# Kernel tuning notes

Measured on AMD Instinct MI355X. Metric: run time of the kernel, lower is better.

The kernel has to match this reference:

```python
import jax, jax.numpy as jnp
import numpy as np

NUM_LATENTS = 1
NUM_EMBEDDINGS = 2048
EMBEDDING_DIM = 64
DECAY = 0.99
EPS = 1e-5


def setup_inputs() -> dict:
    key = jax.random.key(0)
    k1, k2 = jax.random.split(key)
    x = jax.random.normal(k1, (65536, NUM_LATENTS * EMBEDDING_DIM), dtype=jnp.float32)
    embedding = jax.random.normal(k2, (NUM_LATENTS, NUM_EMBEDDINGS, EMBEDDING_DIM), dtype=jnp.float32)
    cluster_size = jnp.ones((NUM_LATENTS, NUM_EMBEDDINGS), dtype=jnp.float32)
    return {"input": x, "embedding": embedding, "cluster_size": cluster_size}


def reference(input, embedding, cluster_size):
    L, K, D = embedding.shape
    flat = input.reshape(-1, L, D)  # (N, L, D)
    # Squared euclidean distances (N, L, K), expanded form of (x - e)^2 sum over D
    x_sq = jnp.sum(flat * flat, axis=-1, keepdims=True)           # (N, L, 1)
    e_sq = jnp.sum(embedding * embedding, axis=-1)[None]          # (1, L, K)
    cross = jnp.einsum('nld,lkd->nlk', flat, embedding)           # (N, L, K)
    distances = x_sq - 2.0 * cross + e_sq
    encoding_indices = jnp.argmin(distances, axis=-1)             # (N, L)
    # decode: gather codebook vectors
    quantized = embedding[jnp.arange(L)[None, :], encoding_indices]  # (N, L, D)
    encodings = jax.nn.one_hot(encoding_indices, K, dtype=input.dtype)  # (N, L, K)
    # --- EMA update (training branch, non-simple, laplace smoothing) ---
    onehot_sum = jnp.sum(encodings, axis=0)                       # (L, K)
    dw = jnp.einsum('nlk,nld->lkd', encodings, flat)              # (L, K, D)
    new_cluster_size = DECAY * cluster_size + (1.0 - DECAY) * onehot_sum
    n = jnp.sum(new_cluster_size, axis=-1, keepdims=True)
    cs = (new_cluster_size + EPS) / (n + K * EPS) * n
    new_embedding = DECAY * embedding + (1.0 - DECAY) * (dw / cs[..., None])
    # --- losses / outputs ---
    q = quantized.reshape(input.shape)
    commitment_loss = jnp.mean((q - input) ** 2)
    quantized_st = input + jax.lax.stop_gradient(q - input)
    avg_probs = jnp.mean(encodings, axis=0)                       # (L, K)
    perplexity = jnp.exp(-jnp.sum(avg_probs * jnp.log(avg_probs + 1e-10) / L))
    return (quantized_st, encodings, commitment_loss, perplexity, new_embedding, new_cluster_size)
```

## Files before the change

kernel.cpp:

```cpp
#include <hip/hip_runtime.h>
#include <math.h>

#define NROWS 65536
#define KEMB  2048
#define DIM   64
#define DECAYF 0.99f
#define OMDF   0.01f
#define EPSF   1e-5f

#define WS_DW    0
#define WS_CNT   131072
#define WS_LOSS  133120
#define WS_ESQ   133632
#define WS_IDX   135680

#define OUT_Q    0
#define OUT_ENC  4194304
#define OUT_LOSS 138412032
#define OUT_PERP 138412033
#define OUT_NE   138412034
#define OUT_NCS  138543106

typedef float f32x4 __attribute__((ext_vector_type(4)));
typedef float f32x2 __attribute__((ext_vector_type(2)));

__global__ __launch_bounds__(256) void k0_prep(const float* __restrict__ E,
                                               float* __restrict__ ws) {
    int g = blockIdx.x * 256 + threadIdx.x;
    if (g == 0) ws[WS_LOSS] = 0.f;
    ((float4*)(ws + WS_DW))[g] = make_float4(0.f, 0.f, 0.f, 0.f);
    if (g < KEMB) {
        ((unsigned int*)ws)[WS_CNT + g] = 0u;
        const float4* e4 = (const float4*)(E + (size_t)g * DIM);
        float s0 = 0.f, s1 = 0.f, s2 = 0.f, s3 = 0.f;
#pragma unroll
        for (int j = 0; j < 16; j++) {
            float4 v = e4[j];
            s0 = fmaf(v.x, v.x, s0); s1 = fmaf(v.y, v.y, s1);
            s2 = fmaf(v.z, v.z, s2); s3 = fmaf(v.w, v.w, s3);
        }
        ws[WS_ESQ + g] = (s0 + s1) + (s2 + s3);
    }
}

__global__ __launch_bounds__(256, 2) void k1_main(const float* __restrict__ x,
                                                  const float* __restrict__ E,
                                                  float* __restrict__ ws,
                                                  float* __restrict__ out) {
    __shared__ float sxT[64 * 128];
    __shared__ float seT[32 * 256];
    __shared__ float sxq[256];

    const int t = threadIdx.x;
    const int b = blockIdx.x;
    const int tx = t & 15;
    const int ty = t >> 4;

    {
        const int rl = t & 127;
        const int dhi2 = t >> 7;
        const float4* x4 = (const float4*)x;
        float s0 = 0.f, s1 = 0.f, s2 = 0.f, s3 = 0.f;
#pragma unroll
        for (int i = 0; i < 8; i++) {
            int dc = dhi2 + 2 * i;
            float4 v = x4[((size_t)b * 128 + rl) * 16 + dc];
            sxT[(4 * dc + 0) * 128 + rl] = v.x;
            sxT[(4 * dc + 1) * 128 + rl] = v.y;
            sxT[(4 * dc + 2) * 128 + rl] = v.z;
            sxT[(4 * dc + 3) * 128 + rl] = v.w;
            s0 = fmaf(v.x, v.x, s0); s1 = fmaf(v.y, v.y, s1);
            s2 = fmaf(v.z, v.z, s2); s3 = fmaf(v.w, v.w, s3);
        }
        sxq[dhi2 * 128 + rl] = (s0 + s1) + (s2 + s3);
    }

    const int sbase = (((t >> 2) & 3) << 6) + ((t >> 4) << 2) + (t & 3);
    const float4* e4 = (const float4*)E;

    float4 pv[8];
#pragma unroll
    for (int j = 0; j < 8; j++)
        pv[j] = e4[(size_t)t * 16 + j];

    __syncthreads();

    float xsq[8];
#pragma unroll
    for (int rr = 0; rr < 8; rr++)
        xsq[rr] = sxq[ty * 8 + rr] + sxq[128 + ty * 8 + rr];

    float best[8];
    int bidx[8];
#pragma unroll
    for (int rr = 0; rr < 8; rr++) { best[rr] = 3.4e38f; bidx[rr] = 0; }

    f32x4* __restrict__ encz = (f32x4*)(out + OUT_ENC);

    for (int pass = 0; pass < 8; pass++) {
        f32x2 acc[8][8];
#pragma unroll
        for (int rr = 0; rr < 8; rr++)
#pragma unroll
            for (int p = 0; p < 8; p++) acc[rr][p] = (f32x2)(0.f);

        for (int dh = 0; dh < 2; dh++) {
            if (pass + dh) __syncthreads();
#pragma unroll
            for (int j = 0; j < 8; j++) {
                seT[(4 * j + 0) * 256 + sbase] = pv[j].x;
                seT[(4 * j + 1) * 256 + sbase] = pv[j].y;
                seT[(4 * j + 2) * 256 + sbase] = pv[j].z;
                seT[(4 * j + 3) * 256 + sbase] = pv[j].w;
            }
            __syncthreads();

            {
                int h = pass * 2 + dh + 1;
                if (h < 16) {
#pragma unroll
                    for (int j = 0; j < 8; j++)
                        pv[j] = e4[((size_t)((h >> 1) * 256 + t)) * 16 + (h & 1) * 8 + j];
                }
            }

            if (dh == 0) {
                f32x4 z = (f32x4)(0.f);
#pragma unroll
                for (int j = 0; j < 32; j++)
                    __builtin_nontemporal_store(z,
                        encz + (size_t)b * 65536 + pass * 8192 + j * 256 + t);
            }

            const float* xbase = sxT + dh * 32 * 128 + ty * 8;
            for (int dd = 0; dd < 32; dd++) {
                const float* sb = seT + dd * 256;
                f32x4 a0 = *(const f32x4*)(xbase + dd * 128);
                f32x4 a1 = *(const f32x4*)(xbase + dd * 128 + 4);
                f32x4 b0 = *(const f32x4*)(sb + tx * 4);
                f32x4 b1 = *(const f32x4*)(sb + 64 + tx * 4);
                f32x4 b2 = *(const f32x4*)(sb + 128 + tx * 4);
                f32x4 b3 = *(const f32x4*)(sb + 192 + tx * 4);
                f32x2 bp[8];
                bp[0] = __builtin_shufflevector(b0, b0, 0, 1);
                bp[1] = __builtin_shufflevector(b0, b0, 2, 3);
                bp[2] = __builtin_shufflevector(b1, b1, 0, 1);
                bp[3] = __builtin_shufflevector(b1, b1, 2, 3);
                bp[4] = __builtin_shufflevector(b2, b2, 0, 1);
                bp[5] = __builtin_shufflevector(b2, b2, 2, 3);
                bp[6] = __builtin_shufflevector(b3, b3, 0, 1);
                bp[7] = __builtin_shufflevector(b3, b3, 2, 3);
#pragma unroll
                for (int rr = 0; rr < 4; rr++) {
                    f32x2 al = (f32x2)(a0[rr]);
                    f32x2 ah = (f32x2)(a1[rr]);
#pragma unroll
                    for (int p = 0; p < 8; p++) {
                        acc[rr][p]     = __builtin_elementwise_fma(al, bp[p], acc[rr][p]);
                        acc[rr + 4][p] = __builtin_elementwise_fma(ah, bp[p], acc[rr + 4][p]);
                    }
                }
            }
        }

        const float4* esq4 = (const float4*)(ws + WS_ESQ + pass * 256 + tx * 16);
        float4 eqv0 = esq4[0], eqv1 = esq4[1], eqv2 = esq4[2], eqv3 = esq4[3];
        float eq[16] = {eqv0.x, eqv0.y, eqv0.z, eqv0.w, eqv1.x, eqv1.y, eqv1.z, eqv1.w,
                        eqv2.x, eqv2.y, eqv2.z, eqv2.w, eqv3.x, eqv3.y, eqv3.z, eqv3.w};
        const int kb = pass * 256 + tx * 16;
#pragma unroll
        for (int rr = 0; rr < 8; rr++)
#pragma unroll
            for (int p = 0; p < 8; p++)
#pragma unroll
                for (int e = 0; e < 2; e++) {
                    float dist = fmaf(-2.f, acc[rr][p][e], xsq[rr]) + eq[p * 2 + e];
                    if (dist < best[rr]) { best[rr] = dist; bidx[rr] = kb + p * 2 + e; }
                }
    }

    int* sIdx = (int*)sxq;
#pragma unroll
    for (int rr = 0; rr < 8; rr++) {
        float bd = best[rr]; int bi = bidx[rr];
#pragma unroll
        for (int m = 1; m < 16; m <<= 1) {
            float od = __shfl_xor(bd, m, 64);
            int   oi = __shfl_xor(bi, m, 64);
            if (od < bd || (od == bd && oi < bi)) { bd = od; bi = oi; }
        }
        if (tx == 0) sIdx[ty * 8 + rr] = bi;
    }
    __syncthreads();

    if (t < 128) {
        const int row = b * 128 + t;
        const int bi = sIdx[t];
        ((int*)ws)[WS_IDX + row] = bi;
        out[OUT_ENC + (size_t)row * KEMB + bi] = 1.0f;
        const float4* ebb = (const float4*)(E + (size_t)bi * DIM);
        const float4* xr4 = (const float4*)(x + (size_t)row * DIM);
        float4* qo = (float4*)(out + OUT_Q + (size_t)row * DIM);
        float l0 = 0.f, l1 = 0.f, l2 = 0.f, l3 = 0.f;
#pragma unroll
        for (int j = 0; j < 16; j++) {
            float4 ev = ebb[j];
            float4 xv = xr4[j];
            qo[j] = ev;
            float d0 = ev.x - xv.x, d1 = ev.y - xv.y;
            float d2 = ev.z - xv.z, d3 = ev.w - xv.w;
            l0 = fmaf(d0, d0, l0); l1 = fmaf(d1, d1, l1);
            l2 = fmaf(d2, d2, l2); l3 = fmaf(d3, d3, l3);
        }
        float lsum = (l0 + l1) + (l2 + l3);
#pragma unroll
        for (int o = 32; o; o >>= 1) lsum += __shfl_down(lsum, o, 64);
        if ((t & 63) == 0) unsafeAtomicAdd(ws + WS_LOSS, lsum);
    }
}

__global__ __launch_bounds__(256) void k2_dwD(const float* __restrict__ x,
                                              const int* __restrict__ idxp,
                                              float* __restrict__ ws) {
    __shared__ float tab[4][2056];
    __shared__ unsigned int htab[KEMB];
    const int t = threadIdx.x;
    const int b = blockIdx.x;
    const int d0 = (b & 15) * 4;
    const int rbase = (b >> 4) * 2048;
    const bool counting = (b & 15) == 0;

#pragma unroll
    for (int j = 0; j < 33; j++) {
        int p = t + j * 256;
        if (p < 4 * 2056) ((float*)tab)[p] = 0.f;
    }
    if (counting) {
#pragma unroll
        for (int j = 0; j < 8; j++) htab[t + j * 256] = 0u;
    }
    __syncthreads();

    const int rt = t >> 2;
    const int dsub = t & 3;
#pragma unroll 8
    for (int i = 0; i < 32; i++) {
        int row = rbase + i * 64 + rt;
        int code = idxp[row];
        float v = x[(size_t)row * DIM + d0 + dsub];
        atomicAdd(&tab[dsub][code], v);
        if (counting && dsub == 0) atomicAdd(&htab[code], 1u);
    }
    __syncthreads();

#pragma unroll
    for (int dl = 0; dl < 4; dl++)
#pragma unroll
        for (int j2 = 0; j2 < 8; j2++) {
            int k = t + j2 * 256;
            float v = tab[dl][k];
            if (v != 0.f)
                unsafeAtomicAdd(ws + WS_DW + (size_t)(d0 + dl) * KEMB + k, v);
        }
    if (counting) {
#pragma unroll
        for (int j = 0; j < 8; j++) {
            int k = t + j * 256;
            unsigned int v = htab[k];
            if (v) atomicAdd(((unsigned int*)ws) + WS_CNT + k, v);
        }
    }
}

__global__ __launch_bounds__(256) void k3_se(const float* __restrict__ cs_in,
                                             const float* __restrict__ E,
                                             const float* __restrict__ ws,
                                             float* __restrict__ out) {
    __shared__ float sred[8];
    __shared__ float sscale[16];
    __shared__ float s_n;
    const int t = threadIdx.x;
    const int b = blockIdx.x;
    const unsigned int* cnt = ((const unsigned int*)ws) + WS_CNT;

    float ln = 0.f, lent = 0.f;
#pragma unroll
    for (int j = 0; j < 8; j++) {
        int k = t * 8 + j;
        float c = (float)cnt[k];
        float ncs = DECAYF * cs_in[k] + OMDF * c;
        ln += ncs;
        float p = c * (1.0f / 65536.0f);
        lent = fmaf(p, logf(p + 1e-10f), lent);
    }
#pragma unroll
    for (int o = 32; o; o >>= 1) {
        ln += __shfl_down(ln, o, 64);
        lent += __shfl_down(lent, o, 64);
    }
    if ((t & 63) == 0) { sred[t >> 6] = ln; sred[4 + (t >> 6)] = lent; }
    __syncthreads();
    if (t == 0) {
        float n = (sred[0] + sred[1]) + (sred[2] + sred[3]);
        float ent = (sred[4] + sred[5]) + (sred[6] + sred[7]);
        s_n = n;
        if (b == 0) {
            out[OUT_LOSS] = ws[WS_LOSS] * (1.0f / 4194304.0f);
            out[OUT_PERP] = expf(-ent);
        }
    }
    __syncthreads();
    const float n = s_n;

    if (t < 16) {
        int k = b * 16 + t;
        float c = (float)cnt[k];
        float ncs = DECAYF * cs_in[k] + OMDF * c;
        out[OUT_NCS + k] = ncs;
        float cs = (ncs + EPSF) / (n + (float)KEMB * EPSF) * n;
        sscale[t] = OMDF / cs;
    }
    __syncthreads();

    const int kk = b * 16 + (t & 15);
    const int d4 = t >> 4;
    const float sc = sscale[t & 15];
    float dv0 = ws[WS_DW + (size_t)(d4 * 4 + 0) * KEMB + kk];
    float dv1 = ws[WS_DW + (size_t)(d4 * 4 + 1) * KEMB + kk];
    float dv2 = ws[WS_DW + (size_t)(d4 * 4 + 2) * KEMB + kk];
    float dv3 = ws[WS_DW + (size_t)(d4 * 4 + 3) * KEMB + kk];
    float4 e = ((const float4*)E)[kk * 16 + d4];
    float2 r0, r1;
    r0.x = fmaf(dv0, sc, DECAYF * e.x);
    r0.y = fmaf(dv1, sc, DECAYF * e.y);
    r1.x = fmaf(dv2, sc, DECAYF * e.z);
    r1.y = fmaf(dv3, sc, DECAYF * e.w);
    float2* o2 = (float2*)(out + OUT_NE);
    o2[(kk * 64 + d4 * 4) / 2 + 0] = r0;
    o2[(kk * 64 + d4 * 4) / 2 + 1] = r1;
}

extern "C" void kernel_launch(void* const* d_in, const int* in_sizes, int n_in,
                              void* d_out, int out_size, void* d_ws, size_t ws_size,
                              hipStream_t stream) {
    const float* x = (const float*)d_in[0];
    const float* E = (const float*)d_in[1];
    const float* cs = (const float*)d_in[2];
    float* out = (float*)d_out;
    float* ws = (float*)d_ws;
    const int* idxp = ((const int*)ws) + WS_IDX;

    hipLaunchKernelGGL(k0_prep, dim3(128), dim3(256), 0, stream, E, ws);
    hipLaunchKernelGGL(k1_main, dim3(512), dim3(256), 0, stream, x, E, ws, out);
    hipLaunchKernelGGL(k2_dwD, dim3(512), dim3(256), 0, stream, x, idxp, ws);
    hipLaunchKernelGGL(k3_se, dim3(128), dim3(256), 0, stream, cs, E, ws, out);
}
```

Measured before the change: 276.9 us.

## Double-buffer codebook chunks in shared memory with one barrier per chunk

Splits each 256-code pass into four 16-dim chunks held in two shared-memory buffers. The next chunk is written to the alternate buffer while the current one is consumed, which leaves one barrier per chunk instead of two. Prefetch registers drop from 8 to 4 float4 and shared memory per block stays the same. The one-hot zero stores are also spread across the chunks. In exchange there are more barriers in total and shorter inner loops.

```diff
diff --git a/kernel.cpp b/kernel.cpp
--- a/kernel.cpp
+++ b/kernel.cpp
@@ -48,7 +48,7 @@
                                                   float* __restrict__ ws,
                                                   float* __restrict__ out) {
     __shared__ float sxT[64 * 128];
-    __shared__ float seT[32 * 256];
+    __shared__ float seT[2][16 * 256];
     __shared__ float sxq[256];
 
     const int t = threadIdx.x;
@@ -78,10 +78,20 @@
     const int sbase = (((t >> 2) & 3) << 6) + ((t >> 4) << 2) + (t & 3);
     const float4* e4 = (const float4*)E;
 
-    float4 pv[8];
-#pragma unroll
-    for (int j = 0; j < 8; j++)
+    float4 pv[4];
+#pragma unroll
+    for (int j = 0; j < 4; j++)
         pv[j] = e4[(size_t)t * 16 + j];
+#pragma unroll
+    for (int j = 0; j < 4; j++) {
+        seT[0][(4 * j + 0) * 256 + sbase] = pv[j].x;
+        seT[0][(4 * j + 1) * 256 + sbase] = pv[j].y;
+        seT[0][(4 * j + 2) * 256 + sbase] = pv[j].z;
+        seT[0][(4 * j + 3) * 256 + sbase] = pv[j].w;
+    }
+#pragma unroll
+    for (int j = 0; j < 4; j++)
+        pv[j] = e4[(size_t)t * 16 + 4 + j];
 
     __syncthreads();
 
@@ -104,37 +114,38 @@
 #pragma unroll
             for (int p = 0; p < 8; p++) acc[rr][p] = (f32x2)(0.f);
 
-        for (int dh = 0; dh < 2; dh++) {
-            if (pass + dh) __syncthreads();
-#pragma unroll
-            for (int j = 0; j < 8; j++) {
-                seT[(4 * j + 0) * 256 + sbase] = pv[j].x;
-                seT[(4 * j + 1) * 256 + sbase] = pv[j].y;
-                seT[(4 * j + 2) * 256 + sbase] = pv[j].z;
-                seT[(4 * j + 3) * 256 + sbase] = pv[j].w;
-            }
-            __syncthreads();
-
-            {
-                int h = pass * 2 + dh + 1;
-                if (h < 16) {
-#pragma unroll
-                    for (int j = 0; j < 8; j++)
-                        pv[j] = e4[((size_t)((h >> 1) * 256 + t)) * 16 + (h & 1) * 8 + j];
+        for (int q = 0; q < 4; q++) {
+            const int s = pass * 4 + q;
+            const int buf = s & 1;
+
+            if (s < 31) {
+#pragma unroll
+                for (int j = 0; j < 4; j++) {
+                    seT[buf ^ 1][(4 * j + 0) * 256 + sbase] = pv[j].x;
+                    seT[buf ^ 1][(4 * j + 1) * 256 + sbase] = pv[j].y;
+                    seT[buf ^ 1][(4 * j + 2) * 256 + sbase] = pv[j].z;
+                    seT[buf ^ 1][(4 * j + 3) * 256 + sbase] = pv[j].w;
                 }
             }
-
-            if (dh == 0) {
+            if (s < 30) {
+                int h = s + 2;
+#pragma unroll
+                for (int j = 0; j < 4; j++)
+                    pv[j] = e4[(size_t)((h >> 2) * 256 + t) * 16 + (h & 3) * 4 + j];
+            }
+
+            {
                 f32x4 z = (f32x4)(0.f);
 #pragma unroll
-                for (int j = 0; j < 32; j++)
+                for (int j = 0; j < 8; j++)
                     __builtin_nontemporal_store(z,
-                        encz + (size_t)b * 65536 + pass * 8192 + j * 256 + t);
+                        encz + (size_t)b * 65536 + s * 2048 + j * 256 + t);
             }
 
-            const float* xbase = sxT + dh * 32 * 128 + ty * 8;
-            for (int dd = 0; dd < 32; dd++) {
-                const float* sb = seT + dd * 256;
+            const float* xbase = sxT + (q * 16) * 128 + ty * 8;
+            const float* sbuf = seT[buf];
+            for (int dd = 0; dd < 16; dd++) {
+                const float* sb = sbuf + dd * 256;
                 f32x4 a0 = *(const f32x4*)(xbase + dd * 128);
                 f32x4 a1 = *(const f32x4*)(xbase + dd * 128 + 4);
                 f32x4 b0 = *(const f32x4*)(sb + tx * 4);
@@ -161,6 +172,7 @@
                     }
                 }
             }
+            __syncthreads();
         }
 
         const float4* esq4 = (const float4*)(ws + WS_ESQ + pass * 256 + tx * 16);
```

Measured after the change: 275.8 us. About the same (-0.4%).
